# Kernel tuning notes

Hardware: AMD Instinct MI355X
Metric: run time of the kernel (lower is better)

## Reference

```python
import jax, jax.numpy as jnp
import numpy as np

B, T, M, H = 256, 64, 256, 256


def setup_inputs() -> dict:
    key = jax.random.key(0)
    ks = jax.random.split(key, 16)
    n = jax.random.normal
    s = 0.05  # small init so tanh/sigmoid stay in sane range
    return {
        "enc_inputs": n(ks[0], (T, B, M), jnp.float32),  # module transposes (0,1) itself
        "y": n(ks[1], (B, T, 1), jnp.float32),
        "W_d": n(ks[2], (M, 2 * H), jnp.float32) * s,
        "b_Wd": n(ks[3], (M,), jnp.float32) * s,
        "U_d": n(ks[4], (M, M), jnp.float32) * s,
        "v_d": n(ks[5], (1, M), jnp.float32) * s,
        "w_tilda": n(ks[6], (1, M + 1), jnp.float32) * s,
        "b_wt": n(ks[7], (1,), jnp.float32) * s,
        "W_ih": n(ks[8], (4 * H, 1), jnp.float32) * s,
        "W_hh": n(ks[9], (4 * H, H), jnp.float32) * s,
        "b_ih": n(ks[10], (4 * H,), jnp.float32) * s,
        "b_hh": n(ks[11], (4 * H,), jnp.float32) * s,
        "W_y": n(ks[12], (H, H + M), jnp.float32) * s,
        "b_Wy": n(ks[13], (H,), jnp.float32) * s,
        "v_y": n(ks[14], (1, H), jnp.float32) * s,
        "b_vy": n(ks[15], (1,), jnp.float32) * s,
    }


def reference(enc_inputs, y, W_d, b_Wd, U_d, v_d, w_tilda, b_wt,
              W_ih, W_hh, b_ih, b_hh, W_y, b_Wy, v_y, b_vy):
    enc = jnp.swapaxes(enc_inputs, 0, 1)                 # (B,T,M)
    # U_d(enc) is loop-invariant; hoist (same math as recomputing per step)
    y1 = jnp.einsum('btm,nm->btn', enc, U_d)             # (B,T,M)
    ys = jnp.swapaxes(y, 0, 1)                           # (T,B,1) scanned over time
    b = enc.shape[0]
    d0 = jnp.zeros((b, H), enc.dtype)
    s0 = jnp.zeros((b, H), enc.dtype)
    c0 = jnp.zeros((b, M), enc.dtype)

    def step(carry, y_t):
        d, sp, _ = carry
        # Bahdanau-style temporal attention over encoder steps
        x1 = jnp.concatenate([d, sp], axis=1) @ W_d.T + b_Wd      # (B,M)
        l = jnp.tanh(x1[:, None, :] + y1) @ v_d[0]                # (B,T)
        beta = jax.nn.softmax(l, axis=1)
        c = jnp.einsum('bt,btm->bm', beta, enc)                   # (B,M)
        # scalar driving input for the decoder LSTM cell
        y_til = jnp.concatenate([c, y_t], axis=1) @ w_tilda.T + b_wt  # (B,1)
        # torch.nn.LSTMCell update with (h, c) = (d, sp)
        gates = y_til @ W_ih.T + b_ih + d @ W_hh.T + b_hh         # (B,4H)
        i, f, g, o = jnp.split(gates, 4, axis=1)
        sp_new = jax.nn.sigmoid(f) * sp + jax.nn.sigmoid(i) * jnp.tanh(g)
        d_new = jax.nn.sigmoid(o) * jnp.tanh(sp_new)
        return (d_new, sp_new, c), None

    (d, sp, c), _ = jax.lax.scan(step, (d0, s0, c0), ys)
    h = jnp.concatenate([d, c], axis=1) @ W_y.T + b_Wy            # (B,H)
    return h @ v_y.T + b_vy                                        # (B,1)
```

## Files before the change

kernel.cpp:

```cpp
#include <hip/hip_runtime.h>


#define Bx 256
#define Tx 64
#define Mx 256
#define Hx 256
#define NT 1024
#define XS 20

typedef unsigned int  uint;
typedef unsigned short ushort;
typedef _Float16 h2  __attribute__((ext_vector_type(2)));
typedef float    f2v __attribute__((ext_vector_type(2)));

__device__ __forceinline__ float4 ld4(const float* p) { return *(const float4*)p; }
__device__ __forceinline__ float h2f(ushort s) {
  union { ushort s; _Float16 h; } c; c.s = s; return (float)c.h;
}
__device__ __forceinline__ ushort f2h(float f) {
  union { _Float16 h; ushort s; } c; c.h = (_Float16)f; return c.s;
}
__device__ __forceinline__ uint pk2(float a, float b) {
  return (uint)f2h(a) | ((uint)f2h(b) << 16);
}

#if defined(__has_builtin)
#if __has_builtin(__builtin_amdgcn_rcpf)
#define RCPF(x) __builtin_amdgcn_rcpf(x)
#endif
#if __has_builtin(__builtin_amdgcn_fdot2)
#define HAVE_FDOT2 1
#endif
#if __has_builtin(__builtin_amdgcn_cvt_pk_f32_fp8) && __has_builtin(__builtin_amdgcn_cvt_pk_fp8_f32)
#define HAVE_FP8 1
#endif
#endif
#ifndef RCPF
#define RCPF(x) (1.0f / (x))
#endif

__device__ __forceinline__ float tanh_fast(float x) {
  float e2 = __expf(2.0f * x);
  return 1.0f - 2.0f * RCPF(e2 + 1.0f);
}
__device__ __forceinline__ float tanh_pre(float z2) {
  return 1.0f - 2.0f * RCPF(__expf(z2) + 1.0f);
}
__device__ __forceinline__ float sigm(float x) {
  return RCPF(1.0f + __expf(-x));
}
__device__ __forceinline__ float wave_sum(float v) {
  #pragma unroll
  for (int o = 1; o < 64; o <<= 1) v += __shfl_xor(v, o, 64);
  return v;
}
__device__ __forceinline__ int xsw(int m) { return (m >> 4) * XS + (m & 15); }

__device__ __forceinline__ uint sw8(float f) {
  union { float f; uint u; } c; c.f = f;
  uint s = (c.u >> 31) << 7;
  float a = fabsf(f);
  if (!(a >= 0.0009765625f)) return s;
  if (a >= 448.f) return s | 0x7e;
  int e = (int)((c.u >> 23) & 0xff) - 127;
  if (e < -6) { int q = (int)(a * 512.f + 0.5f); return s | (uint)q; }
  uint m = ((c.u & 0x7fffff) + 0x80000) >> 20;
  if (m == 8) { m = 0; ++e; }
  if (e > 8) return s | 0x7e;
  return s | ((uint)(e + 7) << 3) | m;
}
__device__ __forceinline__ float sw8d(uint b) {
  uint s = b >> 7, e = (b >> 3) & 0xf, m = b & 7;
  float v;
  if (e) { union { uint u; float f; } c; c.u = ((e + 120u) << 23) | (m << 20); v = c.f; }
  else v = (float)m * 0.001953125f;
  return s ? -v : v;
}
__device__ __forceinline__ uint pk_fp8x4(float w0, float w1, float w2, float w3) {
#ifdef HAVE_FP8
  int u = 0;
  u = __builtin_amdgcn_cvt_pk_fp8_f32(w0, w1, u, false);
  u = __builtin_amdgcn_cvt_pk_fp8_f32(w2, w3, u, true);
  return (uint)u;
#else
  return sw8(w0) | (sw8(w1) << 8) | (sw8(w2) << 16) | (sw8(w3) << 24);
#endif
}
template <bool HI>
__device__ __forceinline__ f2v dec2(uint w) {
#ifdef HAVE_FP8
  return __builtin_amdgcn_cvt_pk_f32_fp8((int)w, HI);
#else
  uint b0 = HI ? ((w >> 16) & 0xffu) : (w & 0xffu);
  uint b1 = HI ? (w >> 24) : ((w >> 8) & 0xffu);
  return f2v{sw8d(b0), sw8d(b1)};
#endif
}
__device__ __forceinline__ f2v dotq(uint w, float4 a, f2v acc) {
  acc += dec2<false>(w) * f2v{a.x, a.y};
  acc += dec2<true>(w)  * f2v{a.z, a.w};
  return acc;
}

__global__ __launch_bounds__(256)
void pack_weights(const float* __restrict__ W_d,
                  const float* __restrict__ W_hh,
                  const float* __restrict__ U_d,
                  const float* __restrict__ W_y,
                  uint4* __restrict__ Whh8q,
                  uint4* __restrict__ Wd8q,
                  uint4* __restrict__ Ud8,
                  float* __restrict__ Wyt) {
  const int blk = blockIdx.x, tid = threadIdx.x;
  if (blk < 16) {
    const int k16 = blk;
    #pragma unroll
    for (int q = 0; q < 4; ++q) {
      const int j = tid + 256 * q;
      const float* wr = W_hh + (size_t)j * 256 + 16 * k16;
      float4 a = ld4(wr), b = ld4(wr + 4), c = ld4(wr + 8), d = ld4(wr + 12);
      uint4 u;
      u.x = pk_fp8x4(16.f * a.x, 16.f * a.y, 16.f * a.z, 16.f * a.w);
      u.y = pk_fp8x4(16.f * b.x, 16.f * b.y, 16.f * b.z, 16.f * b.w);
      u.z = pk_fp8x4(16.f * c.x, 16.f * c.y, 16.f * c.z, 16.f * c.w);
      u.w = pk_fp8x4(16.f * d.x, 16.f * d.y, 16.f * d.z, 16.f * d.w);
      Whh8q[k16 * 1024 + j] = u;
    }
  } else if (blk < 48) {
    const int k16 = blk - 16;
    const float* wr = W_d + (size_t)tid * 512 + 16 * k16;
    float4 a = ld4(wr), b = ld4(wr + 4), c = ld4(wr + 8), d = ld4(wr + 12);
    uint4 u;
    u.x = pk_fp8x4(16.f * a.x, 16.f * a.y, 16.f * a.z, 16.f * a.w);
    u.y = pk_fp8x4(16.f * b.x, 16.f * b.y, 16.f * b.z, 16.f * b.w);
    u.z = pk_fp8x4(16.f * c.x, 16.f * c.y, 16.f * c.z, 16.f * c.w);
    u.w = pk_fp8x4(16.f * d.x, 16.f * d.y, 16.f * d.z, 16.f * d.w);
    Wd8q[k16 * 256 + tid] = u;
  } else if (blk < 80) {
    const int m8 = blk - 48;
    float4 a = ld4(U_d + (size_t)tid * 256 + 8 * m8);
    float4 b = ld4(U_d + (size_t)tid * 256 + 8 * m8 + 4);
    Ud8[m8 * 256 + tid] = uint4{pk2(2.f * a.x, 2.f * a.y), pk2(2.f * a.z, 2.f * a.w),
                                pk2(2.f * b.x, 2.f * b.y), pk2(2.f * b.z, 2.f * b.w)};
  } else {
    const int k0 = (blk - 80) * 4;
    float4 w = ld4(W_y + (size_t)tid * 512 + k0);
    Wyt[(k0 + 0) * 256 + tid] = w.x;
    Wyt[(k0 + 1) * 256 + tid] = w.y;
    Wyt[(k0 + 2) * 256 + tid] = w.z;
    Wyt[(k0 + 3) * 256 + tid] = w.w;
  }
}

__global__ __launch_bounds__(NT, 1)
void fused(const float* __restrict__ enc,
           const float* __restrict__ yv,
           const float* __restrict__ b_Wd,
           const float* __restrict__ v_d,
           const float* __restrict__ w_tilda,
           const float* __restrict__ b_wt,
           const float* __restrict__ W_ih,
           const float* __restrict__ b_ih,
           const float* __restrict__ b_hh,
           const float* __restrict__ b_Wy,
           const float* __restrict__ v_y,
           const float* __restrict__ b_vy,
           const uint4* __restrict__ Whh8q,
           const uint4* __restrict__ Wd8q,
           const uint4* __restrict__ Ud8,
           const float* __restrict__ Wyt,
           ushort* __restrict__ Y1,
           float* __restrict__ out)
{
  extern __shared__ __align__(16) uint4 wdl[];
  __shared__ __align__(16) float dsp_s[2 * Hx];
  __shared__ __align__(16) float xq_s[2 * 16 * XS];
  __shared__ __align__(16) float vd_s[16 * XS];
  __shared__ float gates_s[1024];
  __shared__ float dcfin_s[2 * Hx];
  __shared__ float l_s[Tx];
  __shared__ uint  beta2_s[Tx / 2];
  __shared__ float e_s[Tx];
  __shared__ float red_s[4];
  __shared__ float ytil_s;
  __shared__ unsigned flagX, flagL;

  const int b   = blockIdx.x;
  const int tid = threadIdx.x;
  const int h   = tid & 255;
  const int p   = tid >> 8;
  const size_t BM = (size_t)Bx * Mx;

  #pragma unroll
  for (int i = 0; i < 8; ++i) wdl[i * NT + tid] = Wd8q[i * NT + tid];
  if (tid < 256) vd_s[xsw(tid)] = v_d[tid];
  if (tid < 512) dsp_s[tid] = 0.0f;
  if (tid == 0) { flagX = 0u; flagL = 0u; }

  float bj0 = 0.f, bj1 = 0.f;
  if (tid < 512) { bj0 = b_ih[tid] + b_hh[tid]; bj1 = b_ih[tid + 512] + b_hh[tid + 512]; }
  float bWd_r = 0.f;
  if (tid >= 512 && tid < 768) bWd_r = 2.0f * b_Wd[tid - 512];
  float wih0 = 0.f, wih1 = 0.f, wih2 = 0.f, wih3 = 0.f;
  if (tid >= 512 && tid < 768) {
    const int hh = tid - 512;
    wih0 = W_ih[hh]; wih1 = W_ih[hh + 256]; wih2 = W_ih[hh + 512]; wih3 = W_ih[hh + 768];
  }
  float yv_r = 0.f;
  if (tid >= 512 && tid < 576) yv_r = yv[b * Tx + (tid - 512)];
  const float wty = w_tilda[Mx];
  const float bwt = b_wt[0];

  if (tid < Tx) {
    const float* er = enc + (size_t)tid * BM + (size_t)b * Mx;
    float acc = 0.0f;
    for (int m = 0; m < Mx; m += 4) {
      float4 e4 = ld4(er + m);
      float4 w4 = ld4(w_tilda + m);
      acc += e4.x * w4.x + e4.y * w4.y + e4.z * w4.z + e4.w * w4.w;
    }
    e_s[tid] = acc;
  }

  {
    const int n = h;
    const float* eb = enc + (size_t)b * Mx;
    for (int tb = p * 16; tb < p * 16 + 16; tb += 8) {
      f2v acc2[8];
      #pragma unroll
      for (int j = 0; j < 8; ++j) acc2[j] = f2v{0.f, 0.f};
      #pragma unroll 2
      for (int m8 = 0; m8 < 32; ++m8) {
        uint4 u = Ud8[m8 * 256 + n];
        f2v w01 = f2v{h2f((ushort)u.x), h2f((ushort)(u.x >> 16))};
        f2v w23 = f2v{h2f((ushort)u.y), h2f((ushort)(u.y >> 16))};
        f2v w45 = f2v{h2f((ushort)u.z), h2f((ushort)(u.z >> 16))};
        f2v w67 = f2v{h2f((ushort)u.w), h2f((ushort)(u.w >> 16))};
        #pragma unroll
        for (int j = 0; j < 8; ++j) {
          const float* ep = eb + (size_t)(tb + j) * BM + 8 * m8;
          float4 ea = ld4(ep), eb4 = ld4(ep + 4);
          acc2[j] += f2v{ea.x, ea.y} * w01;
          acc2[j] += f2v{ea.z, ea.w} * w23;
          acc2[j] += f2v{eb4.x, eb4.y} * w45;
          acc2[j] += f2v{eb4.z, eb4.w} * w67;
        }
      }
      #pragma unroll
      for (int j = 0; j < 8; ++j)
        Y1[((size_t)b * Tx + tb + j) * Mx + n] = f2h(acc2[j].x + acc2[j].y);
    }
  }
  __syncthreads();

  float e_r = 0.0f;
  if (tid >= 512 && tid < 576) e_r = e_s[tid - 512];

  float sp_reg = 0.0f;

  for (int t = 0; t < Tx; ++t) {
    if (tid < 512) {
      f2v ga = f2v{0.f, 0.f}, gb = f2v{0.f, 0.f};
      const uint4* wp = Whh8q + tid;
      #pragma unroll 2
      for (int c = 0; c < 16; ++c) {
        uint4 wa = wp[c * 1024];
        uint4 wb = wp[c * 1024 + 512];
        const float4* ap = (const float4*)dsp_s + 4 * c;
        float4 a0 = ap[0], a1 = ap[1], a2 = ap[2], a3 = ap[3];
        ga = dotq(wa.x, a0, ga); ga = dotq(wa.y, a1, ga);
        ga = dotq(wa.z, a2, ga); ga = dotq(wa.w, a3, ga);
        gb = dotq(wb.x, a0, gb); gb = dotq(wb.y, a1, gb);
        gb = dotq(wb.z, a2, gb); gb = dotq(wb.w, a3, gb);
      }
      gates_s[tid]       = (ga.x + ga.y) * 0.0625f + bj0;
      gates_s[tid + 512] = (gb.x + gb.y) * 0.0625f + bj1;
    } else {
      const int idx = tid - 512;
      const int m = idx & 255, q = idx >> 8;
      const int tq = idx >> 3, lq = idx & 7;
      const ushort* y1r = Y1 + ((size_t)b * Tx + tq) * Mx + lq * 32;
      uint4 yq0 = *(const uint4*)(y1r);
      uint4 yq1 = *(const uint4*)(y1r + 8);
      uint4 yq2 = *(const uint4*)(y1r + 16);
      uint4 yq3 = *(const uint4*)(y1r + 24);
      {
        f2v xa2 = f2v{0.f, 0.f};
        const uint4* xp = wdl + m + (q * 16) * 256;
        #pragma unroll 4
        for (int i = 0; i < 16; ++i) {
          uint4 u = xp[i * 256];
          const float4* ap = (const float4*)dsp_s + 64 * q + 4 * i;
          float4 a0 = ap[0], a1 = ap[1], a2 = ap[2], a3 = ap[3];
          xa2 = dotq(u.x, a0, xa2); xa2 = dotq(u.y, a1, xa2);
          xa2 = dotq(u.z, a2, xa2); xa2 = dotq(u.w, a3, xa2);
        }
        xq_s[q * (16 * XS) + xsw(m)] = (xa2.x + xa2.y) * 0.125f
                                     + (q == 0 ? bWd_r : 0.0f);
      }
      __threadfence_block();
      if ((threadIdx.x & 63) == 0)
        __hip_atomic_fetch_add(&flagX, 1u, __ATOMIC_RELEASE, __HIP_MEMORY_SCOPE_WORKGROUP);
      const unsigned tgtX = 8u * (unsigned)(t + 1);
      while (__hip_atomic_load(&flagX, __ATOMIC_ACQUIRE, __HIP_MEMORY_SCOPE_WORKGROUP) < tgtX) {}

      {
        float ps = 0.0f;
        uint yy[8] = {yq0.x, yq0.y, yq0.z, yq0.w, yq1.x, yq1.y, yq1.z, yq1.w};
        uint zz[8] = {yq2.x, yq2.y, yq2.z, yq2.w, yq3.x, yq3.y, yq3.z, yq3.w};
        #pragma unroll
        for (int g = 0; g < 8; ++g) {
          const int c   = 2 * lq + (g >> 2);
          const int off = c * XS + 4 * (g & 3);
          float4 xa0 = *(const float4*)(xq_s + off);
          float4 xa1 = *(const float4*)(xq_s + 16 * XS + off);
          float4 vv  = *(const float4*)(vd_s + off);
          uint ya = (g < 4) ? yy[2 * g] : zz[2 * (g - 4)];
          uint yb = (g < 4) ? yy[2 * g + 1] : zz[2 * (g - 4) + 1];
          ps += tanh_pre(xa0.x + xa1.x + h2f((ushort)ya)) * vv.x
              + tanh_pre(xa0.y + xa1.y + h2f((ushort)(ya >> 16))) * vv.y
              + tanh_pre(xa0.z + xa1.z + h2f((ushort)yb)) * vv.z
              + tanh_pre(xa0.w + xa1.w + h2f((ushort)(yb >> 16))) * vv.w;
        }
        ps += __shfl_xor(ps, 1, 64);
        ps += __shfl_xor(ps, 2, 64);
        ps += __shfl_xor(ps, 4, 64);
        if (lq == 0) l_s[tq] = ps;
      }
      __threadfence_block();
      if ((threadIdx.x & 63) == 0)
        __hip_atomic_fetch_add(&flagL, 1u, __ATOMIC_RELEASE, __HIP_MEMORY_SCOPE_WORKGROUP);

      if (idx < 64) {
        __builtin_amdgcn_s_setprio(1);
        const unsigned tgtL = 8u * (unsigned)(t + 1);
        while (__hip_atomic_load(&flagL, __ATOMIC_ACQUIRE, __HIP_MEMORY_SCOPE_WORKGROUP) < tgtL) {}
        float e0  = __expf(l_s[idx]);
        float den = e0;
        float num = e0 * e_r;
        #pragma unroll
        for (int o = 1; o < 64; o <<= 1) {
          den += __shfl_xor(den, o, 64);
          num += __shfl_xor(num, o, 64);
        }
        if (t == Tx - 1) {
          float beta = e0 * RCPF(den);
          float bn = __shfl_xor(beta, 1, 64);
          if (!(idx & 1)) beta2_s[idx >> 1] = pk2(beta, bn);
        }
        if (idx == t) ytil_s = num * RCPF(den) + wty * yv_r + bwt;
        __builtin_amdgcn_s_setprio(0);
      }
    }
    __syncthreads();

    if (tid >= 512 && tid < 768) {
      __builtin_amdgcn_s_setprio(1);
      const int hh = tid - 512;
      const float ytil = ytil_s;
      float fi = sigm(gates_s[hh]       + ytil * wih0);
      float ff = sigm(gates_s[256 + hh] + ytil * wih1);
      float fg = tanh_fast(gates_s[512 + hh] + ytil * wih2);
      float fo = sigm(gates_s[768 + hh] + ytil * wih3);
      float spn = ff * sp_reg + fi * fg;
      float dn  = fo * tanh_fast(spn);
      sp_reg = spn;
      dsp_s[hh]       = dn;
      dsp_s[256 + hh] = spn;
      if (t == Tx - 1) dcfin_s[hh] = dn;
      __builtin_amdgcn_s_setprio(0);
    }
    __syncthreads();
  }

  if (tid >= 512) {
    const int idx = tid - 512;
    const int m = idx >> 1, q = idx & 1;
    float acc = 0.0f;
    #pragma unroll 4
    for (int j = 0; j < 32; ++j) {
      const int tt = q * 32 + j;
      uint bp = beta2_s[tt >> 1];
      float bb = (tt & 1) ? h2f((ushort)(bp >> 16)) : h2f((ushort)bp);
      acc += bb * enc[(size_t)tt * BM + (size_t)b * Mx + m];
    }
    acc += __shfl_xor(acc, 1, 64);
    if (q == 0) dcfin_s[256 + m] = acc;
  }
  __syncthreads();

  {
    float a = 0.0f;
    const float* wy = Wyt + h;
    for (int k = 128 * p; k < 128 * p + 128; ++k)
      a += wy[(size_t)k * 256] * dcfin_s[k];
    gates_s[p * 256 + h] = a;
  }
  __syncthreads();
  if (tid < 256) {
    float aa = gates_s[h] + gates_s[256 + h] + gates_s[512 + h] + gates_s[768 + h]
             + b_Wy[h];
    float po = aa * v_y[h];
    po = wave_sum(po);
    if ((tid & 63) == 0) red_s[tid >> 6] = po;
  }
  __syncthreads();
  if (tid == 0) out[b] = red_s[0] + red_s[1] + red_s[2] + red_s[3] + b_vy[0];
}

extern "C" void kernel_launch(void* const* d_in, const int* in_sizes, int n_in,
                              void* d_out, int out_size, void* d_ws, size_t ws_size,
                              hipStream_t stream) {
  const float* enc     = (const float*)d_in[0];
  const float* yv      = (const float*)d_in[1];
  const float* W_d     = (const float*)d_in[2];
  const float* b_Wd    = (const float*)d_in[3];
  const float* U_d     = (const float*)d_in[4];
  const float* v_d     = (const float*)d_in[5];
  const float* w_tilda = (const float*)d_in[6];
  const float* b_wt    = (const float*)d_in[7];
  const float* W_ih    = (const float*)d_in[8];
  const float* W_hh    = (const float*)d_in[9];
  const float* b_ih    = (const float*)d_in[10];
  const float* b_hh    = (const float*)d_in[11];
  const float* W_y     = (const float*)d_in[12];
  const float* b_Wy    = (const float*)d_in[13];
  const float* v_y     = (const float*)d_in[14];
  const float* b_vy    = (const float*)d_in[15];
  float* outp = (float*)d_out;

  char* ws = (char*)d_ws;
  uint4* Whh8q = (uint4*)ws;
  uint4* Wd8q  = (uint4*)(ws + (256 << 10));
  uint4* Ud8   = (uint4*)(ws + (384 << 10));
  float* Wyt   = (float*)(ws + (512 << 10));
  ushort* Y1   = (ushort*)(ws + (1024 << 10));

  const int DYN_LDS = 128 << 10;
  hipFuncSetAttribute((const void*)fused,
                      hipFuncAttributeMaxDynamicSharedMemorySize, DYN_LDS);

  hipLaunchKernelGGL(pack_weights, dim3(208), dim3(256), 0, stream,
                     W_d, W_hh, U_d, W_y, Whh8q, Wd8q, Ud8, Wyt);
  hipLaunchKernelGGL(fused, dim3(Bx), dim3(NT), DYN_LDS, stream,
                     enc, yv, b_Wd, v_d, w_tilda, b_wt, W_ih, b_ih, b_hh,
                     b_Wy, v_y, b_vy, Whh8q, Wd8q, Ud8, Wyt, Y1, outp);
}
```

Before: 594.8 us.

## Replace per-step barrier with flag-based handoff and cache last W_hh chunk in LDS

Removes one __syncthreads per timestep. The LSTM cell update moves to threads 0-255, which keep their own i/g gate values in registers and spin on a workgroup-scope counter. Waves 4-7 and the softmax wave increment that counter after writing their gate partials and ytil. It also stages the last of the 16 W_hh chunks in an extra 16 KB of LDS so that slice is read from LDS instead of global memory each step. The costs are spin-waiting on threads that also compute gates and a larger dynamic LDS allocation.

```diff
diff --git a/kernel.cpp b/kernel.cpp
--- a/kernel.cpp
+++ b/kernel.cpp
@@ -172,7 +172,9 @@
            ushort* __restrict__ Y1,
            float* __restrict__ out)
 {
-  extern __shared__ __align__(16) uint4 wdl[];
+  extern __shared__ __align__(16) uint4 dynls[];
+  uint4* wdl = dynls;
+  uint4* whl = dynls + 8192;
   __shared__ __align__(16) float dsp_s[2 * Hx];
   __shared__ __align__(16) float xq_s[2 * 16 * XS];
   __shared__ __align__(16) float vd_s[16 * XS];
@@ -183,7 +185,7 @@
   __shared__ float e_s[Tx];
   __shared__ float red_s[4];
   __shared__ float ytil_s;
-  __shared__ unsigned flagX, flagL;
+  __shared__ unsigned flagX, flagL, flagE;
 
   const int b   = blockIdx.x;
   const int tid = threadIdx.x;
@@ -193,18 +195,18 @@
 
   #pragma unroll
   for (int i = 0; i < 8; ++i) wdl[i * NT + tid] = Wd8q[i * NT + tid];
+  whl[tid] = Whh8q[15 * 1024 + tid];
   if (tid < 256) vd_s[xsw(tid)] = v_d[tid];
   if (tid < 512) dsp_s[tid] = 0.0f;
-  if (tid == 0) { flagX = 0u; flagL = 0u; }
+  if (tid == 0) { flagX = 0u; flagL = 0u; flagE = 0u; }
 
   float bj0 = 0.f, bj1 = 0.f;
   if (tid < 512) { bj0 = b_ih[tid] + b_hh[tid]; bj1 = b_ih[tid + 512] + b_hh[tid + 512]; }
   float bWd_r = 0.f;
   if (tid >= 512 && tid < 768) bWd_r = 2.0f * b_Wd[tid - 512];
   float wih0 = 0.f, wih1 = 0.f, wih2 = 0.f, wih3 = 0.f;
-  if (tid >= 512 && tid < 768) {
-    const int hh = tid - 512;
-    wih0 = W_ih[hh]; wih1 = W_ih[hh + 256]; wih2 = W_ih[hh + 512]; wih3 = W_ih[hh + 768];
+  if (tid < 256) {
+    wih0 = W_ih[tid]; wih1 = W_ih[tid + 256]; wih2 = W_ih[tid + 512]; wih3 = W_ih[tid + 768];
   }
   float yv_r = 0.f;
   if (tid >= 512 && tid < 576) yv_r = yv[b * Tx + (tid - 512)];
@@ -259,11 +261,12 @@
   float sp_reg = 0.0f;
 
   for (int t = 0; t < Tx; ++t) {
+    float gi = 0.0f, gg = 0.0f;
     if (tid < 512) {
       f2v ga = f2v{0.f, 0.f}, gb = f2v{0.f, 0.f};
       const uint4* wp = Whh8q + tid;
       #pragma unroll 2
-      for (int c = 0; c < 16; ++c) {
+      for (int c = 0; c < 15; ++c) {
         uint4 wa = wp[c * 1024];
         uint4 wb = wp[c * 1024 + 512];
         const float4* ap = (const float4*)dsp_s + 4 * c;
@@ -273,8 +276,25 @@
         gb = dotq(wb.x, a0, gb); gb = dotq(wb.y, a1, gb);
         gb = dotq(wb.z, a2, gb); gb = dotq(wb.w, a3, gb);
       }
-      gates_s[tid]       = (ga.x + ga.y) * 0.0625f + bj0;
-      gates_s[tid + 512] = (gb.x + gb.y) * 0.0625f + bj1;
+      {
+        uint4 wa = whl[tid];
+        uint4 wb = whl[tid + 512];
+        const float4* ap = (const float4*)dsp_s + 60;
+        float4 a0 = ap[0], a1 = ap[1], a2 = ap[2], a3 = ap[3];
+        ga = dotq(wa.x, a0, ga); ga = dotq(wa.y, a1, ga);
+        ga = dotq(wa.z, a2, ga); ga = dotq(wa.w, a3, ga);
+        gb = dotq(wb.x, a0, gb); gb = dotq(wb.y, a1, gb);
+        gb = dotq(wb.z, a2, gb); gb = dotq(wb.w, a3, gb);
+      }
+      gi = (ga.x + ga.y) * 0.0625f + bj0;
+      gg = (gb.x + gb.y) * 0.0625f + bj1;
+      if (tid >= 256) {
+        gates_s[tid]       = gi;
+        gates_s[tid + 512] = gg;
+        __threadfence_block();
+        if ((tid & 63) == 0)
+          __hip_atomic_fetch_add(&flagE, 1u, __ATOMIC_RELEASE, __HIP_MEMORY_SCOPE_WORKGROUP);
+      }
     } else {
       const int idx = tid - 512;
       const int m = idx & 255, q = idx >> 8;
@@ -349,25 +369,28 @@
           if (!(idx & 1)) beta2_s[idx >> 1] = pk2(beta, bn);
         }
         if (idx == t) ytil_s = num * RCPF(den) + wty * yv_r + bwt;
+        __threadfence_block();
+        if (idx == 0)
+          __hip_atomic_fetch_add(&flagE, 1u, __ATOMIC_RELEASE, __HIP_MEMORY_SCOPE_WORKGROUP);
         __builtin_amdgcn_s_setprio(0);
       }
     }
-    __syncthreads();
-
-    if (tid >= 512 && tid < 768) {
+
+    if (tid < 256) {
+      const unsigned tgtE = 5u * (unsigned)(t + 1);
+      while (__hip_atomic_load(&flagE, __ATOMIC_ACQUIRE, __HIP_MEMORY_SCOPE_WORKGROUP) < tgtE) {}
       __builtin_amdgcn_s_setprio(1);
-      const int hh = tid - 512;
       const float ytil = ytil_s;
-      float fi = sigm(gates_s[hh]       + ytil * wih0);
-      float ff = sigm(gates_s[256 + hh] + ytil * wih1);
-      float fg = tanh_fast(gates_s[512 + hh] + ytil * wih2);
-      float fo = sigm(gates_s[768 + hh] + ytil * wih3);
+      float fi = sigm(gi                  + ytil * wih0);
+      float ff = sigm(gates_s[256 + tid]  + ytil * wih1);
+      float fg = tanh_fast(gg             + ytil * wih2);
+      float fo = sigm(gates_s[768 + tid]  + ytil * wih3);
       float spn = ff * sp_reg + fi * fg;
       float dn  = fo * tanh_fast(spn);
       sp_reg = spn;
-      dsp_s[hh]       = dn;
-      dsp_s[256 + hh] = spn;
-      if (t == Tx - 1) dcfin_s[hh] = dn;
+      dsp_s[tid]       = dn;
+      dsp_s[256 + tid] = spn;
+      if (t == Tx - 1) dcfin_s[tid] = dn;
       __builtin_amdgcn_s_setprio(0);
     }
     __syncthreads();
@@ -436,7 +459,7 @@
   float* Wyt   = (float*)(ws + (512 << 10));
   ushort* Y1   = (ushort*)(ws + (1024 << 10));
 
-  const int DYN_LDS = 128 << 10;
+  const int DYN_LDS = (128 + 16) << 10;
   hipFuncSetAttribute((const void*)fused,
                       hipFuncAttributeMaxDynamicSharedMemorySize, DYN_LDS);
 
```

Result: no change. 598.2 us (+0.6%).
